# Kernel optimization log

Hardware: AMD Instinct MI355X
Metric: run time of the kernel (lower is better)

## Reference

```python
import jax, jax.numpy as jnp
import numpy as np

B, T, L = 256, 1024, 64
INIT = 0.1


def setup_inputs() -> dict:
    key = jax.random.key(0)
    k1, k2, k3, k4, k5 = jax.random.split(key, 5)
    scores = jax.random.normal(k1, (B, T, L), dtype=jnp.float32)
    targets = jax.random.randint(k2, (B, T), 0, L)
    start = jax.random.uniform(k3, (L,), dtype=jnp.float32, minval=-INIT, maxval=INIT)
    T_mat = jax.random.uniform(k4, (L, L), dtype=jnp.float32, minval=-INIT, maxval=INIT)
    end = jax.random.uniform(k5, (L,), dtype=jnp.float32, minval=-INIT, maxval=INIT)
    return {"scores": scores, "targets": targets, "start": start, "T_mat": T_mat, "end": end}


def reference(scores, targets, start, T_mat, end):
    # scores: [B,T,L], targets: [B,T] int, start/end: [L], T_mat: [L,L] with T_mat[cur, prev]
    Ttr = T_mat.T  # [prev, cur]

    # --- normalizers via forward algorithm (scan over time) ---
    prev0 = start[None, :] + scores[:, 0]  # [B,L]

    def step(prev, emit):  # prev [B,L], emit [B,L]
        cur = prev[:, :, None] + emit[:, None, :] + Ttr[None, :, :]  # [B,prev,cur]
        return jax.scipy.special.logsumexp(cur, axis=1), None

    emits_t = jnp.swapaxes(scores, 0, 1)[1:]  # [T-1,B,L]
    prev, _ = jax.lax.scan(step, prev0, emits_t)
    normalizers = jax.scipy.special.logsumexp(prev + end[None, :], axis=1)  # [B]

    # --- gold path score ---
    emits = jnp.take_along_axis(scores, targets[:, :, None], axis=2).squeeze(2).sum(axis=1)  # [B]
    trans = (start[targets[:, 0]]
             + T_mat[targets[:, 1:], targets[:, :-1]].sum(axis=1)
             + end[targets[:, -1]])  # [B]
    target_scores = emits + trans

    return (normalizers - target_scores).mean()
```

## Files before the change

kernel.cpp:

```cpp
#include <hip/hip_runtime.h>

#define NB 256
#define NT 1024
#define NL 64

typedef __fp16 h2v __attribute__((ext_vector_type(2)));

__device__ __forceinline__ float rfl_f(float v) {
  return __builtin_bit_cast(float, __builtin_amdgcn_readfirstlane(__builtin_bit_cast(int, v)));
}

__device__ __forceinline__ float dpp_xor1(float v) {
  int i = __builtin_bit_cast(int, v);
  int r = __builtin_amdgcn_update_dpp(i, i, 0xB1, 0xF, 0xF, false);
  return __builtin_bit_cast(float, r);
}

#define DOT4(P, B)                                                            \
  s0 = __builtin_amdgcn_fdot2(__builtin_bit_cast(h2v, (P).x), Rh[(B) + 0], s0, false); \
  s1 = __builtin_amdgcn_fdot2(__builtin_bit_cast(h2v, (P).y), Rh[(B) + 1], s1, false); \
  s2 = __builtin_amdgcn_fdot2(__builtin_bit_cast(h2v, (P).z), Rh[(B) + 2], s2, false); \
  s3 = __builtin_amdgcn_fdot2(__builtin_bit_cast(h2v, (P).w), Rh[(B) + 3], s3, false);

#define CRF_STEP(EF)                                                          \
  do {                                                                        \
    float wn = dpp_xor1(w);                                                   \
    h2v pk = __builtin_amdgcn_cvt_pkrtz(w, wn);                               \
    lb[wslot] = __builtin_bit_cast(int, pk);                                  \
    int4 P0 = lbv[0], P1 = lbv[1], P2 = lbv[2], P3 = lbv[3];                  \
    int4 P4 = lbv[4], P5 = lbv[5], P6 = lbv[6], P7 = lbv[7];                  \
    int e5 = (P0.x >> 10) & 0x1f;                                             \
    float K = __builtin_bit_cast(float, (130 - e5) << 23);                    \
    float KE = K * (EF);                                                      \
    e2 += e5 - 3;                                                             \
    float s0 = 0.f, s1 = 0.f, s2 = 0.f, s3 = 0.f;                             \
    DOT4(P0, 0); DOT4(P1, 4); DOT4(P2, 8); DOT4(P3, 12);                      \
    DOT4(P4, 16); DOT4(P5, 20); DOT4(P6, 24); DOT4(P7, 28);                   \
    w = ((s0 + s1) + (s2 + s3)) * KE;                                         \
  } while (0)

__global__ __launch_bounds__(64) void fb_kernel(const float* __restrict__ scores,
                                                const int* __restrict__ targets,
                                                const float* __restrict__ start,
                                                const float* __restrict__ Tm,
                                                const float* __restrict__ endv,
                                                float* __restrict__ wsA,
                                                float* __restrict__ wsB,
                                                float* __restrict__ wsG) {
  const int lane = threadIdx.x;
  const int bb = blockIdx.x;

  if (bb >= 2 * NB) {
    const int b = bb - 2 * NB;
    const int* tg = targets + b * NT;
    const float* sc = scores + (size_t)b * NT * NL;
    float acc = 0.f;
    for (int t = lane; t < NT; t += 64) {
      int c = tg[t];
      acc += sc[t * NL + c];
      if (t > 0) acc += Tm[c * NL + tg[t - 1]];
    }
#pragma unroll
    for (int off = 32; off > 0; off >>= 1) acc += __shfl_xor(acc, off, 64);
    if (lane == 0) wsG[b] = acc + start[tg[0]] + endv[tg[NT - 1]];
    return;
  }

  __shared__ int4 lbv_s[16];
  int* lb = (int*)lbv_s;
  const int4* lbv = lbv_s;
  const int wslot = (lane & 1) * 32 + (lane >> 1);

  const bool bwd = bb >= NB;
  const int b = bwd ? bb - NB : bb;
  const float* sc = scores + (size_t)b * NT * NL;
  const float LN2 = 0.69314718055994530942f;

  const float* Tb = bwd ? (Tm + lane) : (Tm + lane * NL);
  const int str = bwd ? NL : 1;
  h2v Rh[32];
#pragma unroll
  for (int k = 0; k < 32; k++)
    Rh[k] = __builtin_amdgcn_cvt_pkrtz(__expf(Tb[(2 * k) * str]),
                                       __expf(Tb[(2 * k + 1) * str]));

  if (!bwd) {
    float a0 = start[lane] + sc[lane];
    float m0 = rfl_f(a0);
    float w = __expf(a0 - m0) * 16.f;
    int e2 = -4;

    float buf[4];
#pragma unroll
    for (int k = 0; k < 4; k++) buf[k] = sc[(1 + k) * NL + lane];

    for (int i = 0; i < 128; i++) {
      float nb4[4];
      int tb = 5 + 4 * i;
#pragma unroll
      for (int k = 0; k < 4; k++) nb4[k] = sc[(tb + k) * NL + lane];
      float Ev[4];
#pragma unroll
      for (int k = 0; k < 4; k++) Ev[k] = __expf(buf[k]);
      CRF_STEP(Ev[0]);
      CRF_STEP(Ev[1]);
      CRF_STEP(Ev[2]);
      CRF_STEP(Ev[3]);
#pragma unroll
      for (int k = 0; k < 4; k++) buf[k] = nb4[k];
    }
    wsA[lane * NB + b] = m0 + (float)e2 * LN2 + __logf(w);
  } else {
    float a0 = endv[lane] + sc[(NT - 1) * NL + lane];
    float m0 = rfl_f(a0);
    float w = __expf(a0 - m0) * 16.f;
    int e2 = -4;

    float buf[4];
#pragma unroll
    for (int k = 0; k < 4; k++) buf[k] = sc[(1022 - k) * NL + lane];

    for (int i = 0; i < 127; i++) {
      float nb4[4];
      int tb = 1018 - 4 * i;
#pragma unroll
      for (int k = 0; k < 4; k++) nb4[k] = sc[(tb - k) * NL + lane];
      float Ev[4];
#pragma unroll
      for (int k = 0; k < 4; k++) Ev[k] = __expf(buf[k]);
      CRF_STEP(Ev[0]);
      CRF_STEP(Ev[1]);
      CRF_STEP(Ev[2]);
      CRF_STEP(Ev[3]);
#pragma unroll
      for (int k = 0; k < 4; k++) buf[k] = nb4[k];
    }
    CRF_STEP(__expf(sc[514 * NL + lane]));
    CRF_STEP(__expf(sc[513 * NL + lane]));
    CRF_STEP(1.0f);
    wsB[lane * NB + b] = m0 + (float)e2 * LN2 + __logf(w);
  }
}

__global__ __launch_bounds__(256) void combine_kernel(const float* __restrict__ wsA,
                                                      const float* __restrict__ wsB,
                                                      const float* __restrict__ wsG,
                                                      float* __restrict__ out) {
  const int b = threadIdx.x;
  float m = -INFINITY;
#pragma unroll
  for (int j = 0; j < NL; j++) m = fmaxf(m, wsA[j * NB + b] + wsB[j * NB + b]);
  float s = 0.f;
#pragma unroll
  for (int j = 0; j < NL; j++) s += __expf(wsA[j * NB + b] + wsB[j * NB + b] - m);
  float loss = (m + __logf(s)) - wsG[b];
#pragma unroll
  for (int off = 32; off > 0; off >>= 1) loss += __shfl_xor(loss, off, 64);
  __shared__ float red[4];
  if ((b & 63) == 0) red[b >> 6] = loss;
  __syncthreads();
  if (b == 0) out[0] = (red[0] + red[1] + red[2] + red[3]) * (1.0f / NB);
}

extern "C" void kernel_launch(void* const* d_in, const int* in_sizes, int n_in,
                              void* d_out, int out_size, void* d_ws, size_t ws_size,
                              hipStream_t stream) {
  const float* scores = (const float*)d_in[0];
  const int* targets = (const int*)d_in[1];
  const float* start = (const float*)d_in[2];
  const float* Tm = (const float*)d_in[3];
  const float* endv = (const float*)d_in[4];
  float* out = (float*)d_out;

  float* wsA = (float*)d_ws;
  float* wsB = wsA + NB * NL;
  float* wsG = wsB + NB * NL;

  fb_kernel<<<3 * NB, 64, 0, stream>>>(scores, targets, start, Tm, endv, wsA, wsB, wsG);
  combine_kernel<<<1, 256, 0, stream>>>(wsA, wsB, wsG, out);
}
```

Before: 175.8 us.

## Replace LDS broadcast of CRF state with cross-lane permlane/DPP shuffles

Each recurrence step used to write the packed fp16 state to LDS and read back all 64 values per lane. The new step gathers them with permlane32/permlane16 swaps and a tree of DPP row moves, and permutes the precomputed transition weights per lane so they match the shuffled order. The scale exponent now comes from readfirstlane on lane 0's fp32 value instead of the packed fp16. This removes the LDS round trip and its latency from the serial critical path, at the cost of more VALU/DPP instructions per step.

```diff
diff --git a/kernel.cpp b/kernel.cpp
--- a/kernel.cpp
+++ b/kernel.cpp
@@ -10,32 +10,41 @@
   return __builtin_bit_cast(float, __builtin_amdgcn_readfirstlane(__builtin_bit_cast(int, v)));
 }
 
-__device__ __forceinline__ float dpp_xor1(float v) {
-  int i = __builtin_bit_cast(int, v);
-  int r = __builtin_amdgcn_update_dpp(i, i, 0xB1, 0xF, 0xF, false);
-  return __builtin_bit_cast(float, r);
-}
-
-#define DOT4(P, B)                                                            \
-  s0 = __builtin_amdgcn_fdot2(__builtin_bit_cast(h2v, (P).x), Rh[(B) + 0], s0, false); \
-  s1 = __builtin_amdgcn_fdot2(__builtin_bit_cast(h2v, (P).y), Rh[(B) + 1], s1, false); \
-  s2 = __builtin_amdgcn_fdot2(__builtin_bit_cast(h2v, (P).z), Rh[(B) + 2], s2, false); \
-  s3 = __builtin_amdgcn_fdot2(__builtin_bit_cast(h2v, (P).w), Rh[(B) + 3], s3, false);
+#define DPPI(V, C) __builtin_amdgcn_update_dpp(V, V, C, 0xF, 0xF, false)
 
 #define CRF_STEP(EF)                                                          \
   do {                                                                        \
-    float wn = dpp_xor1(w);                                                   \
-    h2v pk = __builtin_amdgcn_cvt_pkrtz(w, wn);                               \
-    lb[wslot] = __builtin_bit_cast(int, pk);                                  \
-    int4 P0 = lbv[0], P1 = lbv[1], P2 = lbv[2], P3 = lbv[3];                  \
-    int4 P4 = lbv[4], P5 = lbv[5], P6 = lbv[6], P7 = lbv[7];                  \
-    int e5 = (P0.x >> 10) & 0x1f;                                             \
-    float K = __builtin_bit_cast(float, (130 - e5) << 23);                    \
+    int wi = __builtin_bit_cast(int, w);                                      \
+    int e8 = (__builtin_amdgcn_readfirstlane(wi) >> 23) & 0xff;               \
+    float K = __builtin_bit_cast(float, (242 - e8) << 23);                    \
     float KE = K * (EF);                                                      \
-    e2 += e5 - 3;                                                             \
+    e2 += e8 - 115;                                                           \
+    auto u = __builtin_amdgcn_permlane32_swap(wi, wi, false, false);          \
+    auto va = __builtin_amdgcn_permlane16_swap(u[0], u[0], false, false);     \
+    auto vb = __builtin_amdgcn_permlane16_swap(u[1], u[1], false, false);     \
+    int P[32];                                                                \
+    P[0] = __builtin_bit_cast(int, __builtin_amdgcn_cvt_pkrtz(                \
+               __builtin_bit_cast(float, va[0]),                              \
+               __builtin_bit_cast(float, va[1])));                            \
+    P[1] = __builtin_bit_cast(int, __builtin_amdgcn_cvt_pkrtz(                \
+               __builtin_bit_cast(float, vb[0]),                              \
+               __builtin_bit_cast(float, vb[1])));                            \
+    P[2] = DPPI(P[0], 0x140);                            \
+    P[3] = DPPI(P[1], 0x140);                                                 \
+    _Pragma("unroll")                                                         \
+    for (int k = 0; k < 4; k++) P[4 + k] = DPPI(P[k], 0x141);         \
+    _Pragma("unroll")                                                         \
+    for (int k = 0; k < 8; k++) P[8 + k] = DPPI(P[k], 0x1B);          \
+    _Pragma("unroll")                                                         \
+    for (int k = 0; k < 16; k++) P[16 + k] = DPPI(P[k], 0xB1);        \
     float s0 = 0.f, s1 = 0.f, s2 = 0.f, s3 = 0.f;                             \
-    DOT4(P0, 0); DOT4(P1, 4); DOT4(P2, 8); DOT4(P3, 12);                      \
-    DOT4(P4, 16); DOT4(P5, 20); DOT4(P6, 24); DOT4(P7, 28);                   \
+    _Pragma("unroll")                                                         \
+    for (int k = 0; k < 32; k += 4) {                                         \
+      s0 = __builtin_amdgcn_fdot2(__builtin_bit_cast(h2v, P[k + 0]), Rh[k + 0], s0, false); \
+      s1 = __builtin_amdgcn_fdot2(__builtin_bit_cast(h2v, P[k + 1]), Rh[k + 1], s1, false); \
+      s2 = __builtin_amdgcn_fdot2(__builtin_bit_cast(h2v, P[k + 2]), Rh[k + 2], s2, false); \
+      s3 = __builtin_amdgcn_fdot2(__builtin_bit_cast(h2v, P[k + 3]), Rh[k + 3], s3, false); \
+    }                                                                         \
     w = ((s0 + s1) + (s2 + s3)) * KE;                                         \
   } while (0)
 
@@ -66,23 +75,24 @@
     return;
   }
 
-  __shared__ int4 lbv_s[16];
-  int* lb = (int*)lbv_s;
-  const int4* lbv = lbv_s;
-  const int wslot = (lane & 1) * 32 + (lane >> 1);
-
   const bool bwd = bb >= NB;
   const int b = bwd ? bb - NB : bb;
   const float* sc = scores + (size_t)b * NT * NL;
   const float LN2 = 0.69314718055994530942f;
 
+  constexpr int m_seq[16] = {0, 15, 7, 8, 3, 12, 4, 11, 1, 14, 6, 9, 2, 13, 5, 10};
+
   const float* Tb = bwd ? (Tm + lane) : (Tm + lane * NL);
   const int str = bwd ? NL : 1;
   h2v Rh[32];
 #pragma unroll
-  for (int k = 0; k < 32; k++)
-    Rh[k] = __builtin_amdgcn_cvt_pkrtz(__expf(Tb[(2 * k) * str]),
-                                       __expf(Tb[(2 * k + 1) * str]));
+  for (int i = 0; i < 16; i++) {
+    int base = (lane & 15) ^ m_seq[i];
+    Rh[2 * i + 0] = __builtin_amdgcn_cvt_pkrtz(__expf(Tb[(base + 0) * str]),
+                                               __expf(Tb[(base + 16) * str]));
+    Rh[2 * i + 1] = __builtin_amdgcn_cvt_pkrtz(__expf(Tb[(base + 32) * str]),
+                                               __expf(Tb[(base + 48) * str]));
+  }
 
   if (!bwd) {
     float a0 = start[lane] + sc[lane];
```

New measurement: 228.0 us. 1.3x slower.

## Fuse combine kernel into backward blocks via flag-based inter-block sync

Applied to the files above, without the earlier changes.

Drops the separate combine kernel. Each backward block now waits on per-sequence flags set by its matching forward block and the gold-score block, then computes that sequence's logsumexp loss itself. A global atomic counter lets the last block reduce all losses and write the mean. This removes one kernel launch and the serial 256-thread combine tail, but adds a memset launch, spin-waits that assume all 768 blocks are co-resident, and atomic traffic.

```diff
diff --git a/kernel.cpp b/kernel.cpp
--- a/kernel.cpp
+++ b/kernel.cpp
@@ -39,14 +39,22 @@
     w = ((s0 + s1) + (s2 + s3)) * KE;                                         \
   } while (0)
 
+#define AQ __ATOMIC_ACQUIRE
+#define RL __ATOMIC_RELEASE
+#define SCOPE __HIP_MEMORY_SCOPE_AGENT
+
 __global__ __launch_bounds__(64) void fb_kernel(const float* __restrict__ scores,
                                                 const int* __restrict__ targets,
                                                 const float* __restrict__ start,
                                                 const float* __restrict__ Tm,
                                                 const float* __restrict__ endv,
                                                 float* __restrict__ wsA,
-                                                float* __restrict__ wsB,
-                                                float* __restrict__ wsG) {
+                                                float* __restrict__ wsG,
+                                                float* __restrict__ wsL,
+                                                int* __restrict__ flagF,
+                                                int* __restrict__ flagG,
+                                                int* __restrict__ cnt,
+                                                float* __restrict__ out) {
   const int lane = threadIdx.x;
   const int bb = blockIdx.x;
 
@@ -63,6 +71,8 @@
 #pragma unroll
     for (int off = 32; off > 0; off >>= 1) acc += __shfl_xor(acc, off, 64);
     if (lane == 0) wsG[b] = acc + start[tg[0]] + endv[tg[NT - 1]];
+    __threadfence();
+    if (lane == 0) __hip_atomic_store(&flagG[b], 1, RL, SCOPE);
     return;
   }
 
@@ -109,7 +119,9 @@
 #pragma unroll
       for (int k = 0; k < 4; k++) buf[k] = nb4[k];
     }
-    wsA[lane * NB + b] = m0 + (float)e2 * LN2 + __logf(w);
+    wsA[b * NL + lane] = m0 + (float)e2 * LN2 + __logf(w);
+    __threadfence();
+    if (lane == 0) __hip_atomic_store(&flagF[b], 1, RL, SCOPE);
   } else {
     float a0 = endv[lane] + sc[(NT - 1) * NL + lane];
     float m0 = rfl_f(a0);
@@ -138,28 +150,38 @@
     CRF_STEP(__expf(sc[514 * NL + lane]));
     CRF_STEP(__expf(sc[513 * NL + lane]));
     CRF_STEP(1.0f);
-    wsB[lane * NB + b] = m0 + (float)e2 * LN2 + __logf(w);
+    float bv = m0 + (float)e2 * LN2 + __logf(w);
+
+    while (__hip_atomic_load(&flagF[b], AQ, SCOPE) == 0) __builtin_amdgcn_s_sleep(2);
+    float v = wsA[b * NL + lane] + bv;
+    float m = v;
+#pragma unroll
+    for (int off = 32; off > 0; off >>= 1) m = fmaxf(m, __shfl_xor(m, off, 64));
+    float s = __expf(v - m);
+#pragma unroll
+    for (int off = 32; off > 0; off >>= 1) s += __shfl_xor(s, off, 64);
+    while (__hip_atomic_load(&flagG[b], AQ, SCOPE) == 0) __builtin_amdgcn_s_sleep(2);
+    float loss = (m + __logf(s)) - wsG[b];
+
+    int old = -1;
+    if (lane == 0) {
+      wsL[b] = loss;
+      __threadfence();
+      old = __hip_atomic_fetch_add(cnt, 1, __ATOMIC_ACQ_REL, SCOPE);
+    }
+    old = __shfl(old, 0, 64);
+    if (old == NB - 1) {
+      __threadfence();
+      float t0 = __builtin_bit_cast(float, __hip_atomic_load((int*)&wsL[lane], AQ, SCOPE));
+      float t1 = __builtin_bit_cast(float, __hip_atomic_load((int*)&wsL[lane + 64], AQ, SCOPE));
+      float t2 = __builtin_bit_cast(float, __hip_atomic_load((int*)&wsL[lane + 128], AQ, SCOPE));
+      float t3 = __builtin_bit_cast(float, __hip_atomic_load((int*)&wsL[lane + 192], AQ, SCOPE));
+      float tot = (t0 + t1) + (t2 + t3);
+#pragma unroll
+      for (int off = 32; off > 0; off >>= 1) tot += __shfl_xor(tot, off, 64);
+      if (lane == 0) out[0] = tot * (1.0f / NB);
+    }
   }
-}
-
-__global__ __launch_bounds__(256) void combine_kernel(const float* __restrict__ wsA,
-                                                      const float* __restrict__ wsB,
-                                                      const float* __restrict__ wsG,
-                                                      float* __restrict__ out) {
-  const int b = threadIdx.x;
-  float m = -INFINITY;
-#pragma unroll
-  for (int j = 0; j < NL; j++) m = fmaxf(m, wsA[j * NB + b] + wsB[j * NB + b]);
-  float s = 0.f;
-#pragma unroll
-  for (int j = 0; j < NL; j++) s += __expf(wsA[j * NB + b] + wsB[j * NB + b] - m);
-  float loss = (m + __logf(s)) - wsG[b];
-#pragma unroll
-  for (int off = 32; off > 0; off >>= 1) loss += __shfl_xor(loss, off, 64);
-  __shared__ float red[4];
-  if ((b & 63) == 0) red[b >> 6] = loss;
-  __syncthreads();
-  if (b == 0) out[0] = (red[0] + red[1] + red[2] + red[3]) * (1.0f / NB);
 }
 
 extern "C" void kernel_launch(void* const* d_in, const int* in_sizes, int n_in,
@@ -172,10 +194,14 @@
   const float* endv = (const float*)d_in[4];
   float* out = (float*)d_out;
 
-  float* wsA = (float*)d_ws;
-  float* wsB = wsA + NB * NL;
-  float* wsG = wsB + NB * NL;
-
-  fb_kernel<<<3 * NB, 64, 0, stream>>>(scores, targets, start, Tm, endv, wsA, wsB, wsG);
-  combine_kernel<<<1, 256, 0, stream>>>(wsA, wsB, wsG, out);
-}
+  int* flagF = (int*)d_ws;
+  int* flagG = flagF + NB;
+  int* cnt = flagG + NB;
+  float* wsG = (float*)(cnt + 64);
+  float* wsL = wsG + NB;
+  float* wsA = wsL + NB;
+
+  hipMemsetAsync(flagF, 0, (2 * NB + 64) * sizeof(int), stream);
+  fb_kernel<<<3 * NB, 64, 0, stream>>>(scores, targets, start, Tm, endv,
+                                       wsA, wsG, wsL, flagF, flagG, cnt, out);
+}
```

Result: slower. 202.5 us (+15.2%).
